# Kernel tuning notes

Hardware: AMD Instinct MI355X
Metric: run time of the kernel (lower is better)

Reference implementation:

```python
import jax, jax.numpy as jnp
import numpy as np

N = 50000
E = 1_600_000
IN_F = 256
R_IN_F = 8
OUT_F = 128
ALPHA = 0.2  # LeakyReLU negative slope
EPS = 9e-15


def setup_inputs() -> dict:
    key = jax.random.key(0)
    k1, k2, k3, k4, k5, k6, k7 = jax.random.split(key, 7)
    inp = {
        "input": jax.random.normal(k1, (N, IN_F), dtype=jnp.float32),
        "edge_index": jax.random.randint(k2, (2, E), 0, N, dtype=jnp.int64),
        "edge_weight_road": jax.random.uniform(k3, (E,), dtype=jnp.float32),
        "edge_r": jax.random.normal(k4, (E, R_IN_F), dtype=jnp.float32),
        # learned parameters (xavier-normal-like init, gain 1.414)
        "W": jax.random.normal(k5, (IN_F, OUT_F), dtype=jnp.float32)
        * (1.414 * np.sqrt(2.0 / (IN_F + OUT_F))),
        "Wr": jax.random.normal(k6, (R_IN_F, OUT_F), dtype=jnp.float32)
        * (1.414 * np.sqrt(2.0 / (R_IN_F + OUT_F))),
        "a": jax.random.normal(k7, (1, 3 * OUT_F + 1), dtype=jnp.float32)
        * (1.414 * np.sqrt(2.0 / (1 + 3 * OUT_F + 1))),
    }
    return inp


def reference(input, edge_index, edge_weight_road, edge_r, W, Wr, a):
    n = input.shape[0]
    out_f = W.shape[1]
    src, dst = edge_index[0], edge_index[1]

    h = input @ W          # [N, out_f]
    r = edge_r @ Wr        # [E, out_f]

    # a @ cat(h[src], h[dst], r, ew)^T decomposed to avoid materializing [E, 3F+1]
    a_vec = a[0]
    a_src, a_dst, a_r = a_vec[:out_f], a_vec[out_f:2 * out_f], a_vec[2 * out_f:3 * out_f]
    a_w = a_vec[3 * out_f]

    score = (h @ a_src)[src] + (h @ a_dst)[dst] + r @ a_r + a_w * edge_weight_road  # [E]
    edge_e = jnp.exp(-jax.nn.leaky_relu(score, negative_slope=ALPHA))  # [E]

    # sparse [N,N] matmul: out[i] = sum_{edges (i,j)} e_ij * b[j]
    e_rowsum = jax.ops.segment_sum(edge_e, src, num_segments=n)               # [N]
    h_num = jax.ops.segment_sum(edge_e[:, None] * h[dst], src, num_segments=n)  # [N, out_f]

    h_prime = h_num / (e_rowsum[:, None] + EPS)
    return jax.nn.elu(h_prime)  # concat=True
```

## Files before the change

kernel.cpp:

```cpp
#include <hip/hip_runtime.h>

#define IN_F 256
#define OUT_F 128
#define ALPHA 0.2f
#define EPS 9e-15f
#define NBUCK_MAX 512
#define CHUNK 4096
#define LDST 40

typedef __attribute__((ext_vector_type(8))) short bf16x8;
typedef __attribute__((ext_vector_type(4))) float f32x4;

__device__ __forceinline__ unsigned bf16rnd(float f) {
    unsigned b = __float_as_uint(f);
    return b + 0x7FFFu + ((b >> 16) & 1u);
}

__global__ __launch_bounds__(256) void k_conv(const float* __restrict__ W,
                                              unsigned short* __restrict__ Wt) {
    int idx = blockIdx.x * 256 + threadIdx.x;
    if (idx < IN_F * OUT_F) {
        int k = idx >> 7, col = idx & 127;
        Wt[col * IN_F + k] = (unsigned short)(bf16rnd(W[idx]) >> 16);
    }
}

__global__ __launch_bounds__(256) void k_gemm(const float* __restrict__ input,
                                              const unsigned short* __restrict__ Wt,
                                              const float* __restrict__ a,
                                              unsigned short* __restrict__ hb,
                                              float* __restrict__ hs,
                                              float* __restrict__ hd, int n) {
    __shared__ unsigned short Ah[128 * LDST];
    __shared__ unsigned short Al[128 * LDST];
    __shared__ unsigned short Bt[128 * LDST];

    const int t = threadIdx.x;
    const int lane = t & 63;
    const int wave = t >> 6;
    const int l15 = lane & 15;
    const int l4 = lane >> 4;
    const int row0 = blockIdx.x * 128;

    f32x4 acc[2][8];
#pragma unroll
    for (int rt = 0; rt < 2; ++rt)
#pragma unroll
        for (int ct = 0; ct < 8; ++ct) acc[rt][ct] = (f32x4)(0.f);

    for (int ks = 0; ks < 8; ++ks) {
#pragma unroll
        for (int c = t; c < 512; c += 256) {
            int row = c >> 2, kg = c & 3;
            int grow = row0 + row;
            float4 v0 = make_float4(0.f, 0.f, 0.f, 0.f);
            float4 v1 = v0;
            if (grow < n) {
                const float4* src = (const float4*)&input[(size_t)grow * IN_F + ks * 32 + kg * 8];
                v0 = src[0];
                v1 = src[1];
            }
            float xs[8] = {v0.x, v0.y, v0.z, v0.w, v1.x, v1.y, v1.z, v1.w};
            unsigned h[8], l[8];
#pragma unroll
            for (int j = 0; j < 8; ++j) {
                unsigned hbts = bf16rnd(xs[j]) >> 16;
                float hf = __uint_as_float(hbts << 16);
                unsigned lbts = bf16rnd(xs[j] - hf) >> 16;
                h[j] = hbts;
                l[j] = lbts;
            }
            uint4 ph = make_uint4(h[0] | (h[1] << 16), h[2] | (h[3] << 16),
                                  h[4] | (h[5] << 16), h[6] | (h[7] << 16));
            uint4 pl = make_uint4(l[0] | (l[1] << 16), l[2] | (l[3] << 16),
                                  l[4] | (l[5] << 16), l[6] | (l[7] << 16));
            *(uint4*)&Ah[row * LDST + kg * 8] = ph;
            *(uint4*)&Al[row * LDST + kg * 8] = pl;
        }
#pragma unroll
        for (int c = t; c < 512; c += 256) {
            int col = c >> 2, kg = c & 3;
            uint4 v = *(const uint4*)&Wt[col * IN_F + ks * 32 + kg * 8];
            *(uint4*)&Bt[col * LDST + kg * 8] = v;
        }
        __syncthreads();

        bf16x8 a_h[2], a_l[2];
#pragma unroll
        for (int rt = 0; rt < 2; ++rt) {
            int base = (wave * 32 + rt * 16 + l15) * LDST + l4 * 8;
            a_h[rt] = *(bf16x8*)&Ah[base];
            a_l[rt] = *(bf16x8*)&Al[base];
        }
#pragma unroll
        for (int ct = 0; ct < 8; ++ct) {
            bf16x8 b = *(bf16x8*)&Bt[(ct * 16 + l15) * LDST + l4 * 8];
            acc[0][ct] = __builtin_amdgcn_mfma_f32_16x16x32_bf16(a_h[0], b, acc[0][ct], 0, 0, 0);
            acc[0][ct] = __builtin_amdgcn_mfma_f32_16x16x32_bf16(a_l[0], b, acc[0][ct], 0, 0, 0);
            acc[1][ct] = __builtin_amdgcn_mfma_f32_16x16x32_bf16(a_h[1], b, acc[1][ct], 0, 0, 0);
            acc[1][ct] = __builtin_amdgcn_mfma_f32_16x16x32_bf16(a_l[1], b, acc[1][ct], 0, 0, 0);
        }
        __syncthreads();
    }

    float as8[8], ad8[8];
#pragma unroll
    for (int ct = 0; ct < 8; ++ct) {
        as8[ct] = a[ct * 16 + l15];
        ad8[ct] = a[OUT_F + ct * 16 + l15];
    }
#pragma unroll
    for (int rt = 0; rt < 2; ++rt) {
#pragma unroll
        for (int r = 0; r < 4; ++r) {
            int grow = row0 + wave * 32 + rt * 16 + l4 * 4 + r;
            float ps = 0.f, pd = 0.f;
#pragma unroll
            for (int ct = 0; ct < 8; ++ct) {
                float v = acc[rt][ct][r];
                ps = fmaf(v, as8[ct], ps);
                pd = fmaf(v, ad8[ct], pd);
            }
#pragma unroll
            for (int o = 8; o; o >>= 1) {
                ps += __shfl_xor(ps, o);
                pd += __shfl_xor(pd, o);
            }
            if (grow < n) {
#pragma unroll
                for (int ct = 0; ct < 8; ++ct)
                    hb[(size_t)grow * OUT_F + ct * 16 + l15] =
                        (unsigned short)(bf16rnd(acc[rt][ct][r]) >> 16);
                if (l15 == 0) { hs[grow] = ps; hd[grow] = pd; }
            }
        }
    }
}

__global__ __launch_bounds__(256) void k_scanB(const int* __restrict__ bcnt,
                                               int* __restrict__ boffB,
                                               int* __restrict__ bcursor,
                                               int* __restrict__ offs,
                                               int nbuck, int n, int nE) {
    __shared__ int sA[NBUCK_MAX], sB[NBUCK_MAX];
    int t = threadIdx.x;
    for (int i = t; i < NBUCK_MAX; i += 256) sA[i] = (i < nbuck) ? bcnt[i] : 0;
    __syncthreads();
    int *src = sA, *dst = sB;
    for (int ofs = 1; ofs < NBUCK_MAX; ofs <<= 1) {
        for (int i = t; i < NBUCK_MAX; i += 256)
            dst[i] = src[i] + (i >= ofs ? src[i - ofs] : 0);
        __syncthreads();
        int* tmp = src; src = dst; dst = tmp;
    }
    for (int i = t; i < nbuck; i += 256) {
        int ex = i ? src[i - 1] : 0;
        boffB[i] = ex;
        bcursor[i] = ex;
    }
    if (t == 0) offs[n] = nE;
}

__global__ __launch_bounds__(256) void k_edge(const int* __restrict__ ei,
                                              const float* __restrict__ ew,
                                              const float* __restrict__ er,
                                              const float* __restrict__ hs,
                                              const float* __restrict__ hd,
                                              const float* __restrict__ Wr,
                                              const float* __restrict__ a,
                                              float* __restrict__ edge_e,
                                              int* __restrict__ bcnt,
                                              int nE, int n) {
    __shared__ float war[8];
    __shared__ int bh[NBUCK_MAX];
    const int t = threadIdx.x;
    for (int i = t; i < NBUCK_MAX; i += 256) bh[i] = 0;
    {
        int rr = t >> 5;
        int l5 = t & 31;
        float p = 0.f;
#pragma unroll
        for (int k = 0; k < 4; ++k)
            p = fmaf(Wr[rr * OUT_F + l5 * 4 + k], a[2 * OUT_F + l5 * 4 + k], p);
#pragma unroll
        for (int o = 16; o; o >>= 1) p += __shfl_xor(p, o, 32);
        if (l5 == 0) war[rr] = p;
    }
    __syncthreads();

    float aw = a[3 * OUT_F];
    int stride = gridDim.x * 256;
    for (int e = blockIdx.x * 256 + t; e < nE; e += stride) {
        int s = ei[e], d = ei[nE + e];
        s = min(max(s, 0), n - 1);
        d = min(max(d, 0), n - 1);
        float4 r0 = *(const float4*)&er[(size_t)e * 8];
        float4 r1 = *(const float4*)&er[(size_t)e * 8 + 4];
        float sc = hs[s] + hd[d]
                 + r0.x * war[0] + r0.y * war[1] + r0.z * war[2] + r0.w * war[3]
                 + r1.x * war[4] + r1.y * war[5] + r1.z * war[6] + r1.w * war[7]
                 + aw * ew[e];
        float lr = sc > 0.f ? sc : ALPHA * sc;
        edge_e[e] = expf(-lr);
        atomicAdd(&bh[s >> 7], 1);
    }
    __syncthreads();
    int nbuck = (n + 127) >> 7;
    for (int i = t; i < nbuck; i += 256)
        if (bh[i]) atomicAdd(&bcnt[i], bh[i]);
}

__global__ __launch_bounds__(256) void k_bin(const int* __restrict__ ei,
                                             const float* __restrict__ edge_e,
                                             int* __restrict__ bcursor,
                                             int2* __restrict__ binned,
                                             int nE, int n) {
    __shared__ int bcl[NBUCK_MAX];
    __shared__ int gbase[NBUCK_MAX];
    __shared__ unsigned int tmp[CHUNK];
    const int t = threadIdx.x;
    const int base = blockIdx.x * CHUNK;
    for (int i = t; i < NBUCK_MAX; i += 256) bcl[i] = 0;
    __syncthreads();
#pragma unroll
    for (int r = 0; r < CHUNK / 256; ++r) {
        int i = r * 256 + t;
        int e = base + i;
        if (e < nE) {
            int s = ei[e];
            s = min(max(s, 0), n - 1);
            int b = s >> 7;
            int lr = atomicAdd(&bcl[b], 1);
            tmp[i] = ((unsigned)b << 12) | (unsigned)lr | ((unsigned)(s & 127) << 21);
        }
    }
    __syncthreads();
    for (int i = t; i < NBUCK_MAX; i += 256) {
        int c = bcl[i];
        gbase[i] = c ? atomicAdd(&bcursor[i], c) : 0;
    }
    __syncthreads();
#pragma unroll
    for (int r = 0; r < CHUNK / 256; ++r) {
        int i = r * 256 + t;
        int e = base + i;
        if (e < nE) {
            unsigned u = tmp[i];
            int b = (u >> 12) & 0x1FF;
            int lr = u & 4095;
            int sl = (u >> 21) & 127;
            int d = ei[nE + e];
            d = min(max(d, 0), n - 1);
            int2 pr;
            pr.x = (d & 0xFFFF) | (sl << 16);
            pr.y = __float_as_int(edge_e[e]);
            binned[gbase[b] + lr] = pr;
        }
    }
}

__global__ __launch_bounds__(256) void k_sub(const int2* __restrict__ binned,
                                             const int* __restrict__ bcnt,
                                             const int* __restrict__ boffB,
                                             int* __restrict__ offs,
                                             int2* __restrict__ pairs, int n) {
    __shared__ int cnt_l[128];
    __shared__ int sA[128], sB[128];
    __shared__ int cur[128];
    int b = blockIdx.x;
    int t = threadIdx.x;
    int node0 = b << 7;
    if (t < 128) cnt_l[t] = 0;
    __syncthreads();
    int beg = boffB[b], c = bcnt[b];
    for (int i = t; i < c; i += 256) {
        int sl = (binned[beg + i].x >> 16) & 127;
        atomicAdd(&cnt_l[sl], 1);
    }
    __syncthreads();
    if (t < 128) sA[t] = cnt_l[t];
    __syncthreads();
    int *src = sA, *dst = sB;
    for (int ofs = 1; ofs < 128; ofs <<= 1) {
        if (t < 128) dst[t] = src[t] + (t >= ofs ? src[t - ofs] : 0);
        __syncthreads();
        int* tmp = src; src = dst; dst = tmp;
    }
    if (t < 128) {
        int ex = t ? src[t - 1] : 0;
        int node = node0 + t;
        if (node < n) offs[node] = beg + ex;
        cur[t] = ex;
    }
    __syncthreads();
    for (int i = t; i < c; i += 256) {
        int2 pr = binned[beg + i];
        int sl = (pr.x >> 16) & 127;
        int pos = beg + atomicAdd(&cur[sl], 1);
        int2 o;
        o.x = pr.x & 0xFFFF;
        o.y = pr.y;
        pairs[pos] = o;
    }
}

__global__ __launch_bounds__(256) void k_acc(const int2* __restrict__ pairs,
                                             const int* __restrict__ offs,
                                             const unsigned* __restrict__ hb,
                                             float* __restrict__ out, int n) {
    int wid = threadIdx.x >> 6, lane = threadIdx.x & 63;
    int node = blockIdx.x * 4 + wid;
    if (node >= n) return;
    int beg = offs[node], end = offs[node + 1];
    float ax = 0.f, ay = 0.f, rowsum = 0.f;
    int idx = beg;
    for (; idx + 8 <= end; idx += 8) {
        int2 p[8];
        unsigned u[8];
#pragma unroll
        for (int j = 0; j < 8; ++j) p[j] = pairs[idx + j];
#pragma unroll
        for (int j = 0; j < 8; ++j)
            u[j] = hb[(size_t)p[j].x * 64 + lane];
#pragma unroll
        for (int j = 0; j < 8; ++j) {
            float ee = __int_as_float(p[j].y);
            float hx = __uint_as_float(u[j] << 16);
            float hy = __uint_as_float(u[j] & 0xFFFF0000u);
            ax = fmaf(ee, hx, ax);
            ay = fmaf(ee, hy, ay);
            rowsum += ee;
        }
    }
    for (; idx < end; ++idx) {
        int2 p = pairs[idx];
        float ee = __int_as_float(p.y);
        unsigned u = hb[(size_t)p.x * 64 + lane];
        float hx = __uint_as_float(u << 16);
        float hy = __uint_as_float(u & 0xFFFF0000u);
        ax = fmaf(ee, hx, ax);
        ay = fmaf(ee, hy, ay);
        rowsum += ee;
    }
    float inv = 1.f / (rowsum + EPS);
    float x = ax * inv, y = ay * inv;
    x = x > 0.f ? x : (expf(x) - 1.f);
    y = y > 0.f ? y : (expf(y) - 1.f);
    float2 o = make_float2(x, y);
    *(float2*)&out[node * OUT_F + lane * 2] = o;
}

static inline size_t align_up(size_t v, size_t al) { return (v + al - 1) & ~(al - 1); }

extern "C" void kernel_launch(void* const* d_in, const int* in_sizes, int n_in,
                              void* d_out, int out_size, void* d_ws, size_t ws_size,
                              hipStream_t stream) {
    const float* input = (const float*)d_in[0];
    const int*   ei    = (const int*)d_in[1];
    const float* ew    = (const float*)d_in[2];
    const float* er    = (const float*)d_in[3];
    const float* W     = (const float*)d_in[4];
    const float* Wr    = (const float*)d_in[5];
    const float* a     = (const float*)d_in[6];
    float* out = (float*)d_out;

    const int n  = in_sizes[0] / IN_F;
    const int nE = in_sizes[2];
    const int nbuck = (n + 127) >> 7;

    char* p = (char*)d_ws;
    size_t o = 0;
    unsigned short* hb = (unsigned short*)(p + o); o = align_up(o + (size_t)n * OUT_F * 2, 256);
    unsigned short* Wt = (unsigned short*)(p + o); o = align_up(o + (size_t)IN_F * OUT_F * 2, 256);
    float* hs      = (float*)(p + o); o = align_up(o + (size_t)n * 4, 256);
    float* hd      = (float*)(p + o); o = align_up(o + (size_t)n * 4, 256);
    float* edge_e  = (float*)(p + o); o = align_up(o + (size_t)nE * 4, 256);
    int*   offs    = (int*)(p + o);   o = align_up(o + (size_t)(n + 1) * 4, 256);
    int2*  pairs   = (int2*)(p + o);  o = align_up(o + (size_t)nE * 8, 256);
    int2*  binned  = (int2*)(p + o);  o = align_up(o + (size_t)nE * 8, 256);
    int*   bcnt    = (int*)(p + o);   o = align_up(o + NBUCK_MAX * 4, 256);
    int*   boffB   = (int*)(p + o);   o = align_up(o + NBUCK_MAX * 4, 256);
    int*   bcursor = (int*)(p + o);   o = align_up(o + NBUCK_MAX * 4, 256);
    (void)ws_size; (void)n_in; (void)out_size;

    (void)hipMemsetAsync(bcnt, 0, NBUCK_MAX * 4, stream);

    k_conv<<<(IN_F * OUT_F + 255) / 256, 256, 0, stream>>>(W, Wt);
    k_gemm<<<(n + 127) / 128, 256, 0, stream>>>(input, Wt, a, hb, hs, hd, n);
    k_edge<<<1024, 256, 0, stream>>>(ei, ew, er, hs, hd, Wr, a, edge_e,
                                     bcnt, nE, n);
    k_scanB<<<1, 256, 0, stream>>>(bcnt, boffB, bcursor, offs, nbuck, n, nE);
    int nchunk = (nE + CHUNK - 1) / CHUNK;
    k_bin<<<nchunk, 256, 0, stream>>>(ei, edge_e, bcursor, binned, nE, n);
    k_sub<<<nbuck, 256, 0, stream>>>(binned, bcnt, boffB, offs, pairs, n);
    k_acc<<<(n + 3) / 4, 256, 0, stream>>>(pairs, offs, (const unsigned*)hb, out, n);
}
```

Before: 168.6 us.

## Fuse edge score computation into binning kernel, split histogram into light pass

The edge-score computation moves into the binning kernel, and a separate lightweight histogram kernel now only reads source indices to count bucket sizes. This removes the global edge_e array's write and re-read and the second read of destination indices. The cost is a third pass over the source indices, plus about 30KB of extra shared memory per block in the fused kernel, which may reduce occupancy.

```diff
diff --git a/kernel.cpp b/kernel.cpp
--- a/kernel.cpp
+++ b/kernel.cpp
@@ -137,6 +137,25 @@
     }
 }
 
+__global__ __launch_bounds__(256) void k_histB(const int* __restrict__ ei,
+                                               int* __restrict__ bcnt,
+                                               int nE, int n) {
+    __shared__ int bh[NBUCK_MAX];
+    const int t = threadIdx.x;
+    for (int i = t; i < NBUCK_MAX; i += 256) bh[i] = 0;
+    __syncthreads();
+    int stride = gridDim.x * 256;
+    for (int e = blockIdx.x * 256 + t; e < nE; e += stride) {
+        int s = ei[e];
+        s = min(max(s, 0), n - 1);
+        atomicAdd(&bh[s >> 7], 1);
+    }
+    __syncthreads();
+    int nbuck = (n + 127) >> 7;
+    for (int i = t; i < nbuck; i += 256)
+        if (bh[i]) atomicAdd(&bcnt[i], bh[i]);
+}
+
 __global__ __launch_bounds__(256) void k_scanB(const int* __restrict__ bcnt,
                                                int* __restrict__ boffB,
                                                int* __restrict__ bcursor,
@@ -161,20 +180,25 @@
     if (t == 0) offs[n] = nE;
 }
 
-__global__ __launch_bounds__(256) void k_edge(const int* __restrict__ ei,
-                                              const float* __restrict__ ew,
-                                              const float* __restrict__ er,
-                                              const float* __restrict__ hs,
-                                              const float* __restrict__ hd,
-                                              const float* __restrict__ Wr,
-                                              const float* __restrict__ a,
-                                              float* __restrict__ edge_e,
-                                              int* __restrict__ bcnt,
-                                              int nE, int n) {
+__global__ __launch_bounds__(256) void k_edgebin(const int* __restrict__ ei,
+                                                 const float* __restrict__ ew,
+                                                 const float* __restrict__ er,
+                                                 const float* __restrict__ hs,
+                                                 const float* __restrict__ hd,
+                                                 const float* __restrict__ Wr,
+                                                 const float* __restrict__ a,
+                                                 int* __restrict__ bcursor,
+                                                 int2* __restrict__ binned,
+                                                 int nE, int n) {
     __shared__ float war[8];
-    __shared__ int bh[NBUCK_MAX];
+    __shared__ int bcl[NBUCK_MAX];
+    __shared__ int gbase[NBUCK_MAX];
+    __shared__ unsigned int tmp[CHUNK];
+    __shared__ float tmp_ee[CHUNK];
+    __shared__ unsigned short tmp_d[CHUNK];
     const int t = threadIdx.x;
-    for (int i = t; i < NBUCK_MAX; i += 256) bh[i] = 0;
+    const int base = blockIdx.x * CHUNK;
+    for (int i = t; i < NBUCK_MAX; i += 256) bcl[i] = 0;
     {
         int rr = t >> 5;
         int l5 = t & 31;
@@ -188,50 +212,27 @@
     }
     __syncthreads();
 
-    float aw = a[3 * OUT_F];
-    int stride = gridDim.x * 256;
-    for (int e = blockIdx.x * 256 + t; e < nE; e += stride) {
-        int s = ei[e], d = ei[nE + e];
-        s = min(max(s, 0), n - 1);
-        d = min(max(d, 0), n - 1);
-        float4 r0 = *(const float4*)&er[(size_t)e * 8];
-        float4 r1 = *(const float4*)&er[(size_t)e * 8 + 4];
-        float sc = hs[s] + hd[d]
-                 + r0.x * war[0] + r0.y * war[1] + r0.z * war[2] + r0.w * war[3]
-                 + r1.x * war[4] + r1.y * war[5] + r1.z * war[6] + r1.w * war[7]
-                 + aw * ew[e];
-        float lr = sc > 0.f ? sc : ALPHA * sc;
-        edge_e[e] = expf(-lr);
-        atomicAdd(&bh[s >> 7], 1);
-    }
-    __syncthreads();
-    int nbuck = (n + 127) >> 7;
-    for (int i = t; i < nbuck; i += 256)
-        if (bh[i]) atomicAdd(&bcnt[i], bh[i]);
-}
-
-__global__ __launch_bounds__(256) void k_bin(const int* __restrict__ ei,
-                                             const float* __restrict__ edge_e,
-                                             int* __restrict__ bcursor,
-                                             int2* __restrict__ binned,
-                                             int nE, int n) {
-    __shared__ int bcl[NBUCK_MAX];
-    __shared__ int gbase[NBUCK_MAX];
-    __shared__ unsigned int tmp[CHUNK];
-    const int t = threadIdx.x;
-    const int base = blockIdx.x * CHUNK;
-    for (int i = t; i < NBUCK_MAX; i += 256) bcl[i] = 0;
-    __syncthreads();
+    const float aw = a[3 * OUT_F];
 #pragma unroll
     for (int r = 0; r < CHUNK / 256; ++r) {
         int i = r * 256 + t;
         int e = base + i;
         if (e < nE) {
-            int s = ei[e];
+            int s = ei[e], d = ei[nE + e];
             s = min(max(s, 0), n - 1);
+            d = min(max(d, 0), n - 1);
+            float4 r0 = *(const float4*)&er[(size_t)e * 8];
+            float4 r1 = *(const float4*)&er[(size_t)e * 8 + 4];
+            float sc = hs[s] + hd[d]
+                     + r0.x * war[0] + r0.y * war[1] + r0.z * war[2] + r0.w * war[3]
+                     + r1.x * war[4] + r1.y * war[5] + r1.z * war[6] + r1.w * war[7]
+                     + aw * ew[e];
+            float lr = sc > 0.f ? sc : ALPHA * sc;
             int b = s >> 7;
-            int lr = atomicAdd(&bcl[b], 1);
-            tmp[i] = ((unsigned)b << 12) | (unsigned)lr | ((unsigned)(s & 127) << 21);
+            int rank = atomicAdd(&bcl[b], 1);
+            tmp[i] = ((unsigned)b << 12) | (unsigned)rank | ((unsigned)(s & 127) << 21);
+            tmp_ee[i] = expf(-lr);
+            tmp_d[i] = (unsigned short)d;
         }
     }
     __syncthreads();
@@ -247,14 +248,12 @@
         if (e < nE) {
             unsigned u = tmp[i];
             int b = (u >> 12) & 0x1FF;
-            int lr = u & 4095;
+            int rank = u & 4095;
             int sl = (u >> 21) & 127;
-            int d = ei[nE + e];
-            d = min(max(d, 0), n - 1);
             int2 pr;
-            pr.x = (d & 0xFFFF) | (sl << 16);
-            pr.y = __float_as_int(edge_e[e]);
-            binned[gbase[b] + lr] = pr;
+            pr.x = (int)tmp_d[i] | (sl << 16);
+            pr.y = __float_as_int(tmp_ee[i]);
+            binned[gbase[b] + rank] = pr;
         }
     }
 }
@@ -374,7 +373,6 @@
     unsigned short* Wt = (unsigned short*)(p + o); o = align_up(o + (size_t)IN_F * OUT_F * 2, 256);
     float* hs      = (float*)(p + o); o = align_up(o + (size_t)n * 4, 256);
     float* hd      = (float*)(p + o); o = align_up(o + (size_t)n * 4, 256);
-    float* edge_e  = (float*)(p + o); o = align_up(o + (size_t)nE * 4, 256);
     int*   offs    = (int*)(p + o);   o = align_up(o + (size_t)(n + 1) * 4, 256);
     int2*  pairs   = (int2*)(p + o);  o = align_up(o + (size_t)nE * 8, 256);
     int2*  binned  = (int2*)(p + o);  o = align_up(o + (size_t)nE * 8, 256);
@@ -387,11 +385,11 @@
 
     k_conv<<<(IN_F * OUT_F + 255) / 256, 256, 0, stream>>>(W, Wt);
     k_gemm<<<(n + 127) / 128, 256, 0, stream>>>(input, Wt, a, hb, hs, hd, n);
-    k_edge<<<1024, 256, 0, stream>>>(ei, ew, er, hs, hd, Wr, a, edge_e,
-                                     bcnt, nE, n);
+    k_histB<<<1024, 256, 0, stream>>>(ei, bcnt, nE, n);
     k_scanB<<<1, 256, 0, stream>>>(bcnt, boffB, bcursor, offs, nbuck, n, nE);
     int nchunk = (nE + CHUNK - 1) / CHUNK;
-    k_bin<<<nchunk, 256, 0, stream>>>(ei, edge_e, bcursor, binned, nE, n);
+    k_edgebin<<<nchunk, 256, 0, stream>>>(ei, ew, er, hs, hd, Wr, a,
+                                          bcursor, binned, nE, n);
     k_sub<<<nbuck, 256, 0, stream>>>(binned, bcnt, boffB, offs, pairs, n);
     k_acc<<<(n + 3) / 4, 256, 0, stream>>>(pairs, offs, (const unsigned*)hb, out, n);
 }
```

Result: faster. 164.5 us (-2.4%).
